# Kernel tuning notes

Measured on AMD Instinct MI355X. Metric: run time of the kernel, lower is better.

## Reference

```python
import jax, jax.numpy as jnp
import numpy as np

B, S, D, H = 4, 2048, 1024, 16
DEPTH = D // H


def setup_inputs() -> dict:
    key = jax.random.key(0)
    ks = jax.random.split(key, 12)
    inp = {
        'v': jax.random.normal(ks[0], (B, S, D), dtype=jnp.float32),
        'k': jax.random.normal(ks[1], (B, S, D), dtype=jnp.float32),
        'q': jax.random.normal(ks[2], (B, S, D), dtype=jnp.float32),
        # key-padding mask: 1.0 = masked position, 0.0 = attend
        'mask': jax.random.randint(ks[3], (B, 1, 1, S), 0, 2).astype(jnp.float32),
        'Wq': jax.random.normal(ks[4], (D, D), dtype=jnp.float32) / np.sqrt(D),
        'bq': jnp.zeros((D,), dtype=jnp.float32),
        'Wk': jax.random.normal(ks[5], (D, D), dtype=jnp.float32) / np.sqrt(D),
        'bk': jnp.zeros((D,), dtype=jnp.float32),
        'Wv': jax.random.normal(ks[6], (D, D), dtype=jnp.float32) / np.sqrt(D),
        'bv': jnp.zeros((D,), dtype=jnp.float32),
        'Wo': jax.random.normal(ks[7], (D, D), dtype=jnp.float32) / np.sqrt(D),
        'bo': jnp.zeros((D,), dtype=jnp.float32),
    }
    return inp


def _split_heads(x):
    # [B, S, D] -> [B, H, S, depth]
    b, s, _ = x.shape
    return x.reshape(b, s, H, DEPTH).transpose(0, 2, 1, 3)


def reference(v, k, q, mask, Wq, bq, Wk, bk, Wv, bv, Wo, bo):
    qh = _split_heads(q @ Wq + bq)  # [B,H,S,depth]
    kh = _split_heads(k @ Wk + bk)
    vh = _split_heads(v @ Wv + bv)
    logits = jnp.einsum('bhqd,bhkd->bhqk', qh, kh) / jnp.sqrt(
        jnp.asarray(DEPTH, dtype=qh.dtype))
    logits = logits + mask * (-1e9)
    attn = jax.nn.softmax(logits, axis=-1)  # [B,H,Sq,Sk]
    out = jnp.einsum('bhqk,bhkd->bhqd', attn, vh)
    out = out.transpose(0, 2, 1, 3).reshape(q.shape[0], -1, D)  # [B,S,D]
    return out @ Wo + bo
```

## Files before the change

kernel.cpp:

```cpp
#include <hip/hip_runtime.h>
#include <hip/hip_bf16.h>
#include <stdint.h>


#define S_LEN 2048
#define NHEAD 16
#define DEPTH 64
#define DMODEL 1024

typedef __bf16 bf16x8 __attribute__((ext_vector_type(8)));
typedef float f32x4 __attribute__((ext_vector_type(4)));
typedef uint16_t u16x8 __attribute__((ext_vector_type(8)));
typedef uint16_t u16x4 __attribute__((ext_vector_type(4)));

#if __has_builtin(__builtin_amdgcn_exp2f)
#define EXP2F(x) __builtin_amdgcn_exp2f(x)
#else
#define EXP2F(x) __builtin_exp2f(x)
#endif

__device__ __forceinline__ uint16_t f2bf(float x) {
    __hip_bfloat16 h = __float2bfloat16(x);
    union { __hip_bfloat16 h; uint16_t u; } v; v.h = h; return v.u;
}
__device__ __forceinline__ u16x8 pack8(f32x4 a, f32x4 b) {
    u16x8 r;
#pragma unroll
    for (int i = 0; i < 4; ++i) { r[i] = f2bf(a[i]); r[i + 4] = f2bf(b[i]); }
    return r;
}
__device__ __forceinline__ void async16(const void* g, void* l) {
    __builtin_amdgcn_global_load_lds((__attribute__((address_space(1))) void*)(g),
                                     (__attribute__((address_space(3))) void*)(l),
                                     16, 0, 0);
}

__global__ void mask_scan(const float* __restrict__ mask, int* __restrict__ gidx,
                          int* __restrict__ nb) {
    __shared__ int part[256];
    const int b = blockIdx.x, tid = threadIdx.x;
    int flags[8], cnt = 0;
#pragma unroll
    for (int i = 0; i < 8; ++i) {
        flags[i] = (mask[b * S_LEN + tid * 8 + i] == 0.0f) ? 1 : 0;
        cnt += flags[i];
    }
    part[tid] = cnt;
    __syncthreads();
    for (int st = 1; st < 256; st <<= 1) {
        int v = (tid >= st) ? part[tid - st] : 0;
        __syncthreads();
        part[tid] += v;
        __syncthreads();
    }
    int run = part[tid] - cnt;
#pragma unroll
    for (int i = 0; i < 8; ++i) {
        if (flags[i]) { gidx[b * S_LEN + run] = tid * 8 + i; ++run; }
    }
    if (tid == 255) nb[b] = part[255];
}

__global__ void transpose4(const float* __restrict__ w0, const float* __restrict__ w1,
                           const float* __restrict__ w2, const float* __restrict__ w3,
                           uint16_t* __restrict__ dst) {
    __shared__ uint16_t tile[32][33];
    const float* src = (blockIdx.z == 0) ? w0 : (blockIdx.z == 1) ? w1
                     : (blockIdx.z == 2) ? w2 : w3;
    uint16_t* d = dst + (size_t)blockIdx.z * DMODEL * DMODEL;
    int bx = blockIdx.x * 32, by = blockIdx.y * 32;
    int x = threadIdx.x, y0 = threadIdx.y;
#pragma unroll
    for (int i = 0; i < 4; ++i) {
        int y = y0 + i * 8;
        tile[y][x] = f2bf(src[(size_t)(by + y) * DMODEL + bx + x]);
    }
    __syncthreads();
#pragma unroll
    for (int i = 0; i < 4; ++i) {
        int y = y0 + i * 8;
        d[(size_t)(bx + y) * DMODEL + by + x] = tile[x][y];
    }
}

__global__ void zero_tails(const int* __restrict__ nb, uint16_t* __restrict__ Kc,
                           uint16_t* __restrict__ Vc) {
    const int bh = blockIdx.x, b = bh >> 4, t = threadIdx.x;
    const int nbv = nb[b];
    const int end = ((nbv + 63) >> 6) << 6;
    const int tail = end - nbv;
    for (int i = t; i < tail * 64; i += 256) {
        int r = nbv + (i >> 6), c = i & 63;
        Kc[((size_t)bh * S_LEN + r) * DEPTH + c] = 0;
    }
    for (int i = t; i < tail * 64; i += 256) {
        int s = nbv + (i >> 6), d = i & 63;
        int off = s & 63;
        int c1 = ((off & 15) << 2) | (off >> 4);
        int c2 = ((((c1 >> 3) ^ (d & 7)) & 7) << 3) | (c1 & 7);
        Vc[((size_t)bh * DEPTH + d) * S_LEN + (s & ~63) + c2] = 0;
    }
}

__global__ __launch_bounds__(256, 3)
void qkv_gemm(const float* __restrict__ qf, const float* __restrict__ kf,
              const float* __restrict__ vf, const uint16_t* __restrict__ WT4,
              const float* __restrict__ bq, const float* __restrict__ bk,
              const float* __restrict__ bv, uint16_t* __restrict__ Qh,
              uint16_t* __restrict__ Kc, uint16_t* __restrict__ Vc,
              const int* __restrict__ gidx, const int* __restrict__ nb) {
    const int z = blockIdx.z;
    const int fid = blockIdx.x + 8 * blockIdx.y;
    const int n0 = ((fid >> 3) & 7) * 128;
    const int m0 = ((((fid >> 6) << 3)) | (fid & 7)) * 128;
    const int b_ = m0 >> 11;
    int nbv = 0x7FFFFFFF;
    if (z >= 1) {
        nbv = nb[b_];
        if ((m0 & 2047) >= nbv) return;
    }

    __shared__ __align__(16) uint16_t As[2][128 * 32];
    __shared__ __align__(16) uint16_t Bs[2][128 * 32];

    const int t = threadIdx.x;
    const int lane = t & 63, quad = lane >> 4, l16 = lane & 15;
    const int w = t >> 6, wm = w >> 1, wn = w & 1;
    const int K = DMODEL;

    const int r_ld = lane >> 2;
    const int c_ld = (lane & 3) * 8;
    const uint16_t* gB = WT4 + (size_t)z * DMODEL * DMODEL + (size_t)(n0 + r_ld) * K + c_ld;
    const float* bias = (z == 0) ? bq : (z == 1) ? bk : bv;

    const int srow = t >> 1, scol = (t & 1) * 16;
    const float* Af32;
    if (z == 0) {
        Af32 = qf + (size_t)(m0 + srow) * K + scol;
    } else {
        int sp = (m0 & 2047) + srow;
        int rs = (sp < nbv) ? gidx[(b_ << 11) + sp] : 0;
        Af32 = ((z == 1) ? kf : vf) + ((size_t)(b_ << 11) + rs) * K + scol;
    }

    f32x4 acc[4][4];
    const f32x4 z4 = {0.f, 0.f, 0.f, 0.f};
#pragma unroll
    for (int mt = 0; mt < 4; ++mt)
#pragma unroll
        for (int nt = 0; nt < 4; ++nt) acc[mt][nt] = z4;

    f32x4 fa[4];
    auto loadA = [&](int kc) {
#pragma unroll
        for (int i = 0; i < 4; ++i) fa[i] = *(const f32x4*)(Af32 + kc + i * 4);
    };
    uint16_t* wA0 = &As[0][srow * 32 + scol];
    uint16_t* wA1 = &As[1][srow * 32 + scol];
    auto writeA = [&](int buf) {
        uint16_t* d = buf ? wA1 : wA0;
        *(u16x8*)d = pack8(fa[0], fa[1]);
        *(u16x8*)(d + 8) = pack8(fa[2], fa[3]);
    };
    auto issueB = [&](int kc, int buf) {
#pragma unroll
        for (int i = 0; i < 2; ++i) {
            int c = w * 2 + i;
            async16(gB + (size_t)(c * 16) * K + kc, &Bs[buf][c * 512]);
        }
    };
    auto compute = [&](int buf) {
        bf16x8 af[4], bfr[4];
#pragma unroll
        for (int mt = 0; mt < 4; ++mt)
            af[mt] = *(const bf16x8*)&As[buf][(wm * 64 + mt * 16 + l16) * 32 + quad * 8];
#pragma unroll
        for (int nt = 0; nt < 4; ++nt)
            bfr[nt] = *(const bf16x8*)&Bs[buf][(wn * 64 + nt * 16 + l16) * 32 + quad * 8];
#pragma unroll
        for (int mt = 0; mt < 4; ++mt)
#pragma unroll
            for (int nt = 0; nt < 4; ++nt)
                acc[mt][nt] = __builtin_amdgcn_mfma_f32_16x16x32_bf16(af[mt], bfr[nt],
                                                                      acc[mt][nt], 0, 0, 0);
    };

    issueB(0, 0);
    loadA(0);
    writeA(0);
    __builtin_amdgcn_sched_barrier(0);
    loadA(32);
    asm volatile("s_waitcnt vmcnt(4) lgkmcnt(0)" ::: "memory");
    __builtin_amdgcn_s_barrier();
    __builtin_amdgcn_sched_barrier(0);

    for (int s = 0; s < 32; ++s) {
        const int cb = s & 1;
        if (s < 31) issueB((s + 1) * 32, cb ^ 1);
        compute(cb);
        if (s < 31) {
            writeA(cb ^ 1);
            __builtin_amdgcn_sched_barrier(0);
            if (s < 30) {
                loadA((s + 2) * 32);
                __builtin_amdgcn_sched_barrier(0);
                asm volatile("s_waitcnt vmcnt(4) lgkmcnt(0)" ::: "memory");
            } else {
                asm volatile("s_waitcnt vmcnt(0) lgkmcnt(0)" ::: "memory");
            }
            __builtin_amdgcn_s_barrier();
            __builtin_amdgcn_sched_barrier(0);
        }
    }

#pragma unroll
    for (int nt = 0; nt < 4; ++nt) {
        int col = n0 + wn * 64 + nt * 16 + l16;
        float bval = bias[col];
        int h = col >> 6, dp = col & 63;
#pragma unroll
        for (int mt = 0; mt < 4; ++mt) {
#pragma unroll
            for (int r = 0; r < 4; ++r) {
                int row = m0 + wm * 64 + mt * 16 + quad * 4 + r;
                float val = acc[mt][nt][r] + bval;
                int b = row >> 11, s = row & 2047;
                if (z == 0) {
                    Qh[(((size_t)(b * NHEAD + h)) * S_LEN + s) * DEPTH + dp] = f2bf(val);
                } else if (z == 1) {
                    if (s < nbv) {
                        int c2 = ((((dp >> 3) ^ (s & 7)) & 7) << 3) | (dp & 7);
                        Kc[(((size_t)(b * NHEAD + h)) * S_LEN + s) * DEPTH + c2] = f2bf(val);
                    }
                } else {
                    if (s < nbv) {
                        int off = s & 63;
                        int c1 = ((off & 15) << 2) | (off >> 4);
                        int c2 = ((((c1 >> 3) ^ (dp & 7)) & 7) << 3) | (c1 & 7);
                        Vc[(((size_t)(b * NHEAD + h)) * DEPTH + dp) * S_LEN
                           + (s & ~63) + c2] = f2bf(val);
                    }
                }
            }
        }
    }
}

__global__ __launch_bounds__(256, 3)
void out_gemm(const uint16_t* __restrict__ ctx, const uint16_t* __restrict__ Wt,
              const float* __restrict__ bias, float* __restrict__ outp) {
    const int fid = blockIdx.x + 8 * blockIdx.y;
    const int n0 = ((fid >> 3) & 7) * 128;
    const int m0 = ((((fid >> 6) << 3)) | (fid & 7)) * 128;

    __shared__ __align__(16) uint16_t As[2][128 * 32];
    __shared__ __align__(16) uint16_t Bs[2][128 * 32];

    const int t = threadIdx.x;
    const int lane = t & 63, quad = lane >> 4, l16 = lane & 15;
    const int w = t >> 6, wm = w >> 1, wn = w & 1;
    const int K = DMODEL;

    const int r_ld = lane >> 2;
    const int c_ld = (lane & 3) * 8;
    const uint16_t* gB = Wt + (size_t)(n0 + r_ld) * K + c_ld;

    int row0 = m0 + (w * 2 + 0) * 16 + r_ld;
    int row1 = row0 + 16;
    const uint16_t* pA0 = ctx + ((size_t)((row0 >> 11) * NHEAD) * S_LEN + (row0 & 2047)) * DEPTH + c_ld;
    const uint16_t* pA1 = ctx + ((size_t)((row1 >> 11) * NHEAD) * S_LEN + (row1 & 2047)) * DEPTH + c_ld;

    auto stage = [&](int kc, int buf) {
#pragma unroll
        for (int i = 0; i < 2; ++i) {
            int c = w * 2 + i;
            async16(gB + (size_t)(c * 16) * K + kc, &Bs[buf][c * 512]);
        }
        size_t aoff = ((size_t)(kc >> 6) << 17) + (kc & 63);
        async16(pA0 + aoff, &As[buf][(w * 2 + 0) * 512]);
        async16(pA1 + aoff, &As[buf][(w * 2 + 1) * 512]);
    };

    f32x4 acc[4][4];
    const f32x4 z4 = {0.f, 0.f, 0.f, 0.f};
#pragma unroll
    for (int mt = 0; mt < 4; ++mt)
#pragma unroll
        for (int nt = 0; nt < 4; ++nt) acc[mt][nt] = z4;

    stage(0, 0);
    __syncthreads();

    for (int s = 0; s < 32; ++s) {
        const int cb = s & 1;
        if (s < 31) stage((s + 1) * 32, cb ^ 1);
        {
            bf16x8 af[4], bfr[4];
#pragma unroll
            for (int mt = 0; mt < 4; ++mt)
                af[mt] = *(const bf16x8*)&As[cb][(wm * 64 + mt * 16 + l16) * 32 + quad * 8];
#pragma unroll
            for (int nt = 0; nt < 4; ++nt)
                bfr[nt] = *(const bf16x8*)&Bs[cb][(wn * 64 + nt * 16 + l16) * 32 + quad * 8];
#pragma unroll
            for (int mt = 0; mt < 4; ++mt)
#pragma unroll
                for (int nt = 0; nt < 4; ++nt)
                    acc[mt][nt] = __builtin_amdgcn_mfma_f32_16x16x32_bf16(af[mt], bfr[nt],
                                                                          acc[mt][nt], 0, 0, 0);
        }
        if (s < 31) __syncthreads();
    }

#pragma unroll
    for (int nt = 0; nt < 4; ++nt) {
        int col = n0 + wn * 64 + nt * 16 + l16;
        float bval = bias[col];
#pragma unroll
        for (int mt = 0; mt < 4; ++mt) {
#pragma unroll
            for (int r = 0; r < 4; ++r) {
                int row = m0 + wm * 64 + mt * 16 + quad * 4 + r;
                outp[(size_t)row * DMODEL + col] = acc[mt][nt][r] + bval;
            }
        }
    }
}

__global__ __launch_bounds__(256, 3)
void flash_attn(const uint16_t* __restrict__ Qh, const uint16_t* __restrict__ Kc,
                const uint16_t* __restrict__ Vc, const int* __restrict__ nb,
                uint16_t* __restrict__ ctx) {
    __shared__ __align__(16) uint16_t Ks[2][64 * 64];
    __shared__ __align__(16) uint16_t Vs[2][64 * 64];
    __shared__ __align__(16) uint16_t Ps[4][16 * 72];

    const int t = threadIdx.x;
    const int w = t >> 6, lane = t & 63, quad = lane >> 4, l16 = lane & 15;
    const int fid = blockIdx.x + 16 * blockIdx.y;
    const int q0 = ((fid >> 3) & 15) * 128;
    const int bh = ((fid >> 7) << 3) | (fid & 7);
    const int b = bh >> 4;
    const int nbv = nb[b];
    const int ntiles = (nbv + 63) >> 6;

    const int srow8 = lane >> 3, scol8 = (lane & 7) * 8;
    const uint16_t* pKn = Kc + ((size_t)bh * S_LEN + w * 16 + srow8) * DEPTH + scol8;
    const uint16_t* pVn = Vc + ((size_t)bh * DEPTH + w * 16 + srow8) * S_LEN + scol8;
    uint16_t* dK0 = &Ks[0][w * 16 * 64];
    uint16_t* dK1 = &Ks[1][w * 16 * 64];
    uint16_t* dV0 = &Vs[0][w * 16 * 64];
    uint16_t* dV1 = &Vs[1][w * 16 * 64];

    bf16x8 aq[2][2];
#pragma unroll
    for (int mt = 0; mt < 2; ++mt)
#pragma unroll
        for (int kc = 0; kc < 2; ++kc)
            aq[mt][kc] = *(const bf16x8*)(Qh + ((size_t)bh * S_LEN + q0 + w * 32 + mt * 16 + l16) * DEPTH
                                          + kc * 32 + quad * 8);

    float lrow[2][4];
    f32x4 Oacc[2][4];
    const f32x4 z4 = {0.f, 0.f, 0.f, 0.f};
#pragma unroll
    for (int mt = 0; mt < 2; ++mt)
#pragma unroll
        for (int r = 0; r < 4; ++r) lrow[mt][r] = 0.f;
#pragma unroll
    for (int mt = 0; mt < 2; ++mt)
#pragma unroll
        for (int nt = 0; nt < 4; ++nt) Oacc[mt][nt] = z4;

    const float C2 = 0.18033688f;
    const float M2 = 17.312340f;
    const int swzk = l16 & 7;

    async16(pKn, dK0); async16(pKn + 8 * DEPTH, dK0 + 8 * 64);
    async16(pVn, dV0); async16(pVn + 8 * S_LEN, dV0 + 8 * 64);
    pKn += 64 * DEPTH; pVn += 64;
    __syncthreads();

    for (int kt = 0; kt < ntiles; ++kt) {
        const int cur = kt & 1;
        if (kt + 1 < ntiles) {
            uint16_t* dK = cur ? dK0 : dK1;
            uint16_t* dV = cur ? dV0 : dV1;
            async16(pKn, dK); async16(pKn + 8 * DEPTH, dK + 8 * 64);
            async16(pVn, dV); async16(pVn + 8 * S_LEN, dV + 8 * 64);
            pKn += 64 * DEPTH; pVn += 64;
        }
        const uint16_t* ksrc = cur ? &Ks[1][0] : &Ks[0][0];
        const uint16_t* vsrc = cur ? &Vs[1][0] : &Vs[0][0];
        const int k0 = kt * 64;

        float pen[4];
#pragma unroll
        for (int nt = 0; nt < 4; ++nt)
            pen[nt] = (k0 + nt * 16 + l16 < nbv) ? -M2 : -2e9f;

        f32x4 sacc[2][4];
#pragma unroll
        for (int mt = 0; mt < 2; ++mt)
#pragma unroll
            for (int nt = 0; nt < 4; ++nt) sacc[mt][nt] = z4;
        __builtin_amdgcn_s_setprio(1);
#pragma unroll
        for (int kc = 0; kc < 2; ++kc) {
#pragma unroll
            for (int nt = 0; nt < 4; ++nt) {
                bf16x8 bk = *(const bf16x8*)&ksrc[(nt * 16 + l16) * 64 + (((kc * 4 + quad) ^ swzk) << 3)];
#pragma unroll
                for (int mt = 0; mt < 2; ++mt)
                    sacc[mt][nt] = __builtin_amdgcn_mfma_f32_16x16x32_bf16(aq[mt][kc], bk,
                                                                           sacc[mt][nt], 0, 0, 0);
            }
        }
        __builtin_amdgcn_s_setprio(0);

        bf16x8 bvr[2][4];
#pragma unroll
        for (int kc = 0; kc < 2; ++kc)
#pragma unroll
            for (int nt = 0; nt < 4; ++nt)
                bvr[kc][nt] = *(const bf16x8*)&vsrc[(nt * 16 + l16) * 64 + (((kc * 4 + quad) ^ swzk) << 3)];

#pragma unroll
        for (int mt = 0; mt < 2; ++mt) {
#pragma unroll
            for (int r = 0; r < 4; ++r) {
                float p0 = EXP2F(fmaf(sacc[mt][0][r], C2, pen[0]));
                float p1 = EXP2F(fmaf(sacc[mt][1][r], C2, pen[1]));
                float p2 = EXP2F(fmaf(sacc[mt][2][r], C2, pen[2]));
                float p3 = EXP2F(fmaf(sacc[mt][3][r], C2, pen[3]));
                lrow[mt][r] += (p0 + p1) + (p2 + p3);
                u16x4 pk;
                pk[0] = f2bf(p0); pk[1] = f2bf(p1); pk[2] = f2bf(p2); pk[3] = f2bf(p3);
                *(u16x4*)&Ps[w][(quad * 4 + r) * 72 + l16 * 4] = pk;
            }
            __builtin_amdgcn_s_setprio(1);
#pragma unroll
            for (int kc = 0; kc < 2; ++kc) {
                bf16x8 ap = *(const bf16x8*)&Ps[w][l16 * 72 + kc * 32 + quad * 8];
#pragma unroll
                for (int nt = 0; nt < 4; ++nt)
                    Oacc[mt][nt] = __builtin_amdgcn_mfma_f32_16x16x32_bf16(ap, bvr[kc][nt],
                                                                           Oacc[mt][nt], 0, 0, 0);
            }
            __builtin_amdgcn_s_setprio(0);
        }
        __syncthreads();
    }

#pragma unroll
    for (int mt = 0; mt < 2; ++mt) {
#pragma unroll
        for (int r = 0; r < 4; ++r) {
            float rs = lrow[mt][r];
            rs += __shfl_xor(rs, 1);
            rs += __shfl_xor(rs, 2);
            rs += __shfl_xor(rs, 4);
            rs += __shfl_xor(rs, 8);
            float inv = 1.0f / rs;
            int srow = q0 + w * 32 + mt * 16 + quad * 4 + r;
            size_t base = ((size_t)bh * S_LEN + srow) * DEPTH;
#pragma unroll
            for (int nt = 0; nt < 4; ++nt)
                ctx[base + nt * 16 + l16] = f2bf(Oacc[mt][nt][r] * inv);
        }
    }
}

extern "C" void kernel_launch(void* const* d_in, const int* in_sizes, int n_in,
                              void* d_out, int out_size, void* d_ws, size_t ws_size,
                              hipStream_t stream) {
    const float* v    = (const float*)d_in[0];
    const float* k    = (const float*)d_in[1];
    const float* q    = (const float*)d_in[2];
    const float* mask = (const float*)d_in[3];
    const float* Wq   = (const float*)d_in[4];
    const float* bq   = (const float*)d_in[5];
    const float* Wk   = (const float*)d_in[6];
    const float* bk   = (const float*)d_in[7];
    const float* Wv   = (const float*)d_in[8];
    const float* bv   = (const float*)d_in[9];
    const float* Wo   = (const float*)d_in[10];
    const float* bo   = (const float*)d_in[11];

    char* p = (char*)d_ws;
    uint16_t* WT4 = (uint16_t*)p; p += (size_t)4 * DMODEL * DMODEL * 2;
    uint16_t* Qh  = (uint16_t*)p; p += (size_t)64 * S_LEN * DEPTH * 2;
    int* gidx     = (int*)p;      p += (size_t)4 * S_LEN * 4;
    int* nb       = (int*)p;      p += 16;

    uint16_t* Kc = (uint16_t*)d_out;
    uint16_t* Vc = Kc + (size_t)64 * S_LEN * DEPTH;

    mask_scan<<<4, 256, 0, stream>>>(mask, gidx, nb);
    transpose4<<<dim3(32, 32, 4), dim3(32, 8), 0, stream>>>(Wq, Wk, Wv, Wo, WT4);

    qkv_gemm<<<dim3(8, 64, 3), 256, 0, stream>>>(q, k, v, WT4, bq, bk, bv,
                                                 Qh, Kc, Vc, gidx, nb);
    zero_tails<<<64, 256, 0, stream>>>(nb, Kc, Vc);

    flash_attn<<<dim3(16, 64), 256, 0, stream>>>(Qh, Kc, Vc, nb, Qh );

    out_gemm<<<dim3(8, 64), 256, 0, stream>>>(Qh, WT4 + (size_t)3 * DMODEL * DMODEL,
                                              bo, (float*)d_out);
}
```

Before: 330.2 us.

## Deepen GEMM prefetch pipelines to three stages and fully unroll K loops

Both the QKV projection GEMM and the output GEMM move from double to triple buffering. Tiles are prefetched two steps ahead, and the QKV kernel keeps three register sets of fp32 A data in flight. The K loops are fully unrolled with per-step waitcnt values, and MFMA sections are wrapped in s_setprio to favour matrix issue. The A-load mapping in the QKV kernel also changes to two 8-float rows per thread. The aim is to hide global-memory latency behind compute, at the cost of more LDS and registers, which could lower occupancy under launch_bounds(256,3).

```diff
diff --git a/kernel.cpp b/kernel.cpp
--- a/kernel.cpp
+++ b/kernel.cpp
@@ -121,7 +121,7 @@
     }
 
     __shared__ __align__(16) uint16_t As[2][128 * 32];
-    __shared__ __align__(16) uint16_t Bs[2][128 * 32];
+    __shared__ __align__(16) uint16_t Bs[3][128 * 32];
 
     const int t = threadIdx.x;
     const int lane = t & 63, quad = lane >> 4, l16 = lane & 15;
@@ -133,15 +133,21 @@
     const uint16_t* gB = WT4 + (size_t)z * DMODEL * DMODEL + (size_t)(n0 + r_ld) * K + c_ld;
     const float* bias = (z == 0) ? bq : (z == 1) ? bk : bv;
 
-    const int srow = t >> 1, scol = (t & 1) * 16;
-    const float* Af32;
+    const float* pAa;
+    const float* pAb;
     if (z == 0) {
-        Af32 = qf + (size_t)(m0 + srow) * K + scol;
+        pAa = qf + (size_t)(m0 + (t >> 2)) * K + (t & 3) * 8;
+        pAb = pAa + (size_t)64 * K;
     } else {
-        int sp = (m0 & 2047) + srow;
-        int rs = (sp < nbv) ? gidx[(b_ << 11) + sp] : 0;
-        Af32 = ((z == 1) ? kf : vf) + ((size_t)(b_ << 11) + rs) * K + scol;
-    }
+        const float* src = (z == 1) ? kf : vf;
+        int spa = (m0 & 2047) + (t >> 2);
+        int spb = spa + 64;
+        int ra = (spa < nbv) ? gidx[(b_ << 11) + spa] : 0;
+        int rb = (spb < nbv) ? gidx[(b_ << 11) + spb] : 0;
+        pAa = src + ((size_t)(b_ << 11) + ra) * K + (t & 3) * 8;
+        pAb = src + ((size_t)(b_ << 11) + rb) * K + (t & 3) * 8;
+    }
+    asm volatile("" ::: "memory");
 
     f32x4 acc[4][4];
     const f32x4 z4 = {0.f, 0.f, 0.f, 0.f};
@@ -150,68 +156,76 @@
 #pragma unroll
         for (int nt = 0; nt < 4; ++nt) acc[mt][nt] = z4;
 
-    f32x4 fa[4];
-    auto loadA = [&](int kc) {
-#pragma unroll
-        for (int i = 0; i < 4; ++i) fa[i] = *(const f32x4*)(Af32 + kc + i * 4);
-    };
-    uint16_t* wA0 = &As[0][srow * 32 + scol];
-    uint16_t* wA1 = &As[1][srow * 32 + scol];
-    auto writeA = [&](int buf) {
-        uint16_t* d = buf ? wA1 : wA0;
-        *(u16x8*)d = pack8(fa[0], fa[1]);
-        *(u16x8*)(d + 8) = pack8(fa[2], fa[3]);
-    };
-    auto issueB = [&](int kc, int buf) {
-#pragma unroll
-        for (int i = 0; i < 2; ++i) {
-            int c = w * 2 + i;
-            async16(gB + (size_t)(c * 16) * K + kc, &Bs[buf][c * 512]);
-        }
-    };
-    auto compute = [&](int buf) {
-        bf16x8 af[4], bfr[4];
-#pragma unroll
-        for (int mt = 0; mt < 4; ++mt)
-            af[mt] = *(const bf16x8*)&As[buf][(wm * 64 + mt * 16 + l16) * 32 + quad * 8];
-#pragma unroll
-        for (int nt = 0; nt < 4; ++nt)
-            bfr[nt] = *(const bf16x8*)&Bs[buf][(wn * 64 + nt * 16 + l16) * 32 + quad * 8];
-#pragma unroll
-        for (int mt = 0; mt < 4; ++mt)
-#pragma unroll
-            for (int nt = 0; nt < 4; ++nt)
-                acc[mt][nt] = __builtin_amdgcn_mfma_f32_16x16x32_bf16(af[mt], bfr[nt],
-                                                                      acc[mt][nt], 0, 0, 0);
-    };
-
-    issueB(0, 0);
-    loadA(0);
-    writeA(0);
-    __builtin_amdgcn_sched_barrier(0);
-    loadA(32);
-    asm volatile("s_waitcnt vmcnt(4) lgkmcnt(0)" ::: "memory");
+    f32x4 fA0[4], fA1[4], fA2[4];
+
+#define SEL(SET) ((SET) == 0 ? fA0 : (SET) == 1 ? fA1 : fA2)
+#define LOADA(KC, SET) do {                                         \
+        f32x4* c_ = SEL(SET);                                       \
+        c_[0] = *(const f32x4*)(pAa + (KC));                        \
+        c_[1] = *(const f32x4*)(pAa + (KC) + 4);                    \
+        c_[2] = *(const f32x4*)(pAb + (KC));                        \
+        c_[3] = *(const f32x4*)(pAb + (KC) + 4);                    \
+    } while (0)
+#define WRITEA(ABUF, SET) do {                                      \
+        f32x4* c_ = SEL(SET);                                       \
+        uint16_t* d_ = &As[(ABUF)][0] + t * 8;                      \
+        *(u16x8*)d_ = pack8(c_[0], c_[1]);                          \
+        *(u16x8*)(d_ + 2048) = pack8(c_[2], c_[3]);                 \
+    } while (0)
+#define ISSUEB(KC, BBUF) do {                                       \
+        async16(gB + (size_t)((w * 2 + 0) * 16) * K + (KC),         \
+                &Bs[(BBUF)][(w * 2 + 0) * 512]);                    \
+        async16(gB + (size_t)((w * 2 + 1) * 16) * K + (KC),         \
+                &Bs[(BBUF)][(w * 2 + 1) * 512]);                    \
+    } while (0)
+#define COMPUTE(ABUF, BBUF) do {                                    \
+        bf16x8 af[4], bfr[4];                                       \
+        _Pragma("unroll")                                           \
+        for (int mt = 0; mt < 4; ++mt)                              \
+            af[mt] = *(const bf16x8*)&As[(ABUF)][(wm * 64 + mt * 16 + l16) * 32 + quad * 8]; \
+        _Pragma("unroll")                                           \
+        for (int nt = 0; nt < 4; ++nt)                              \
+            bfr[nt] = *(const bf16x8*)&Bs[(BBUF)][(wn * 64 + nt * 16 + l16) * 32 + quad * 8]; \
+        __builtin_amdgcn_s_setprio(1);                              \
+        _Pragma("unroll")                                           \
+        for (int mt = 0; mt < 4; ++mt)                              \
+            _Pragma("unroll")                                       \
+            for (int nt = 0; nt < 4; ++nt)                          \
+                acc[mt][nt] = __builtin_amdgcn_mfma_f32_16x16x32_bf16(af[mt], bfr[nt], \
+                                                                      acc[mt][nt], 0, 0, 0); \
+        __builtin_amdgcn_s_setprio(0);                              \
+    } while (0)
+
+    ISSUEB(0, 0);
+    ISSUEB(32, 1);
+    LOADA(0, 0);
+    LOADA(32, 1);
+    WRITEA(0, 0);
+    LOADA(64, 2);
+    asm volatile("s_waitcnt lgkmcnt(0)" ::: "memory");
     __builtin_amdgcn_s_barrier();
-    __builtin_amdgcn_sched_barrier(0);
-
-    for (int s = 0; s < 32; ++s) {
-        const int cb = s & 1;
-        if (s < 31) issueB((s + 1) * 32, cb ^ 1);
-        compute(cb);
-        if (s < 31) {
-            writeA(cb ^ 1);
-            __builtin_amdgcn_sched_barrier(0);
-            if (s < 30) {
-                loadA((s + 2) * 32);
-                __builtin_amdgcn_sched_barrier(0);
-                asm volatile("s_waitcnt vmcnt(4) lgkmcnt(0)" ::: "memory");
-            } else {
-                asm volatile("s_waitcnt vmcnt(0) lgkmcnt(0)" ::: "memory");
-            }
-            __builtin_amdgcn_s_barrier();
-            __builtin_amdgcn_sched_barrier(0);
-        }
-    }
+
+#define QSTEP(S) do {                                                          \
+        if ((S) + 2 <= 31) ISSUEB(((S) + 2) * 32, ((S) + 2) % 3);              \
+        COMPUTE((S) & 1, (S) % 3);                                             \
+        if ((S) + 1 <= 31) WRITEA(((S) & 1) ^ 1, ((S) + 1) % 3);               \
+        if ((S) + 3 <= 31) LOADA(((S) + 3) * 32, (S) % 3);                     \
+        if ((S) <= 28) {                                                       \
+            asm volatile("s_waitcnt vmcnt(10) lgkmcnt(0)" ::: "memory");       \
+            __builtin_amdgcn_s_barrier();                                      \
+        } else if ((S) == 29) {                                                \
+            asm volatile("s_waitcnt vmcnt(6) lgkmcnt(0)" ::: "memory");        \
+            __builtin_amdgcn_s_barrier();                                      \
+        } else if ((S) == 30) {                                                \
+            asm volatile("s_waitcnt vmcnt(0) lgkmcnt(0)" ::: "memory");        \
+            __builtin_amdgcn_s_barrier();                                      \
+        }                                                                      \
+    } while (0);
+#define QSTEP8(S) QSTEP(S) QSTEP((S)+1) QSTEP((S)+2) QSTEP((S)+3) \
+                  QSTEP((S)+4) QSTEP((S)+5) QSTEP((S)+6) QSTEP((S)+7)
+    QSTEP8(0) QSTEP8(8) QSTEP8(16) QSTEP8(24)
+#undef QSTEP8
+#undef QSTEP
 
 #pragma unroll
     for (int nt = 0; nt < 4; ++nt) {
@@ -244,6 +258,11 @@
             }
         }
     }
+#undef SEL
+#undef LOADA
+#undef WRITEA
+#undef ISSUEB
+#undef COMPUTE
 }
 
 __global__ __launch_bounds__(256, 3)
@@ -253,8 +272,8 @@
     const int n0 = ((fid >> 3) & 7) * 128;
     const int m0 = ((((fid >> 6) << 3)) | (fid & 7)) * 128;
 
-    __shared__ __align__(16) uint16_t As[2][128 * 32];
-    __shared__ __align__(16) uint16_t Bs[2][128 * 32];
+    __shared__ __align__(16) uint16_t As[3][128 * 32];
+    __shared__ __align__(16) uint16_t Bs[3][128 * 32];
 
     const int t = threadIdx.x;
     const int lane = t & 63, quad = lane >> 4, l16 = lane & 15;
@@ -270,16 +289,13 @@
     const uint16_t* pA0 = ctx + ((size_t)((row0 >> 11) * NHEAD) * S_LEN + (row0 & 2047)) * DEPTH + c_ld;
     const uint16_t* pA1 = ctx + ((size_t)((row1 >> 11) * NHEAD) * S_LEN + (row1 & 2047)) * DEPTH + c_ld;
 
-    auto stage = [&](int kc, int buf) {
-#pragma unroll
-        for (int i = 0; i < 2; ++i) {
-            int c = w * 2 + i;
-            async16(gB + (size_t)(c * 16) * K + kc, &Bs[buf][c * 512]);
-        }
-        size_t aoff = ((size_t)(kc >> 6) << 17) + (kc & 63);
-        async16(pA0 + aoff, &As[buf][(w * 2 + 0) * 512]);
-        async16(pA1 + aoff, &As[buf][(w * 2 + 1) * 512]);
-    };
+#define OSTAGE(KC, BUF) do {                                                    \
+        async16(gB + (size_t)((w * 2 + 0) * 16) * K + (KC), &Bs[(BUF)][(w * 2 + 0) * 512]); \
+        async16(gB + (size_t)((w * 2 + 1) * 16) * K + (KC), &Bs[(BUF)][(w * 2 + 1) * 512]); \
+        size_t aoff_ = ((size_t)((KC) >> 6) << 17) + ((KC) & 63);               \
+        async16(pA0 + aoff_, &As[(BUF)][(w * 2 + 0) * 512]);                    \
+        async16(pA1 + aoff_, &As[(BUF)][(w * 2 + 1) * 512]);                    \
+    } while (0)
 
     f32x4 acc[4][4];
     const f32x4 z4 = {0.f, 0.f, 0.f, 0.f};
@@ -288,29 +304,44 @@
 #pragma unroll
         for (int nt = 0; nt < 4; ++nt) acc[mt][nt] = z4;
 
-    stage(0, 0);
-    __syncthreads();
-
-    for (int s = 0; s < 32; ++s) {
-        const int cb = s & 1;
-        if (s < 31) stage((s + 1) * 32, cb ^ 1);
-        {
-            bf16x8 af[4], bfr[4];
-#pragma unroll
-            for (int mt = 0; mt < 4; ++mt)
-                af[mt] = *(const bf16x8*)&As[cb][(wm * 64 + mt * 16 + l16) * 32 + quad * 8];
-#pragma unroll
-            for (int nt = 0; nt < 4; ++nt)
-                bfr[nt] = *(const bf16x8*)&Bs[cb][(wn * 64 + nt * 16 + l16) * 32 + quad * 8];
-#pragma unroll
-            for (int mt = 0; mt < 4; ++mt)
-#pragma unroll
-                for (int nt = 0; nt < 4; ++nt)
-                    acc[mt][nt] = __builtin_amdgcn_mfma_f32_16x16x32_bf16(af[mt], bfr[nt],
-                                                                          acc[mt][nt], 0, 0, 0);
-        }
-        if (s < 31) __syncthreads();
-    }
+    OSTAGE(0, 0);
+    OSTAGE(32, 1);
+    asm volatile("s_waitcnt vmcnt(4) lgkmcnt(0)" ::: "memory");
+    __builtin_amdgcn_s_barrier();
+
+#define OSTEP(S) do {                                                          \
+        {                                                                      \
+            bf16x8 af[4], bfr[4];                                              \
+            _Pragma("unroll")                                                  \
+            for (int mt = 0; mt < 4; ++mt)                                     \
+                af[mt] = *(const bf16x8*)&As[(S) % 3][(wm * 64 + mt * 16 + l16) * 32 + quad * 8]; \
+            _Pragma("unroll")                                                  \
+            for (int nt = 0; nt < 4; ++nt)                                     \
+                bfr[nt] = *(const bf16x8*)&Bs[(S) % 3][(wn * 64 + nt * 16 + l16) * 32 + quad * 8]; \
+            __builtin_amdgcn_s_setprio(1);                                     \
+            _Pragma("unroll")                                                  \
+            for (int mt = 0; mt < 4; ++mt)                                     \
+                _Pragma("unroll")                                              \
+                for (int nt = 0; nt < 4; ++nt)                                 \
+                    acc[mt][nt] = __builtin_amdgcn_mfma_f32_16x16x32_bf16(af[mt], bfr[nt], \
+                                                                          acc[mt][nt], 0, 0, 0); \
+            __builtin_amdgcn_s_setprio(0);                                     \
+        }                                                                      \
+        if ((S) + 2 <= 31) OSTAGE(((S) + 2) * 32, ((S) + 2) % 3);              \
+        if ((S) <= 29) {                                                       \
+            asm volatile("s_waitcnt vmcnt(4) lgkmcnt(0)" ::: "memory");        \
+            __builtin_amdgcn_s_barrier();                                      \
+        } else if ((S) == 30) {                                                \
+            asm volatile("s_waitcnt vmcnt(0) lgkmcnt(0)" ::: "memory");        \
+            __builtin_amdgcn_s_barrier();                                      \
+        }                                                                      \
+    } while (0);
+#define OSTEP8(S) OSTEP(S) OSTEP((S)+1) OSTEP((S)+2) OSTEP((S)+3) \
+                  OSTEP((S)+4) OSTEP((S)+5) OSTEP((S)+6) OSTEP((S)+7)
+    OSTEP8(0) OSTEP8(8) OSTEP8(16) OSTEP8(24)
+#undef OSTEP8
+#undef OSTEP
+#undef OSTAGE
 
 #pragma unroll
     for (int nt = 0; nt < 4; ++nt) {
```

Measured after the change: 312.0 us. -5.5%, faster.
